# Optimization experiments

Hardware: AMD Instinct MI355X
Metric: run time of the kernel (lower is better)

## Reference

```python
import jax, jax.numpy as jnp
import numpy as np

H = 16        # num_heads
D = 128       # head_dim = hidden_size // num_heads
HID = 2048    # hidden_size
BLOCK = 64    # moba_chunk_size
TOPK = 8      # moba_topk


def setup_inputs() -> dict:
    key = jax.random.key(0)
    ks = jax.random.split(key, 5)
    B, S = 1, 2048
    hidden_states = jax.random.normal(ks[0], (B, S, HID), dtype=jnp.float32)
    scale = HID ** -0.5
    Wq = jax.random.normal(ks[1], (HID, H * D), dtype=jnp.float32) * scale
    Wk = jax.random.normal(ks[2], (HID, H * D), dtype=jnp.float32) * scale
    Wv = jax.random.normal(ks[3], (HID, H * D), dtype=jnp.float32) * scale
    Wo = jax.random.normal(ks[4], (H * D, HID), dtype=jnp.float32) * scale
    return {"hidden_states": hidden_states, "Wq": Wq, "Wk": Wk, "Wv": Wv, "Wo": Wo}


def _moba_forward(hidden_states, Wq, Wk, Wv, Wo):
    B, S, _ = hidden_states.shape
    nb = S // BLOCK
    INF = jnp.float32(jnp.inf)

    q = (hidden_states @ Wq).reshape(B, S, H, D)
    k = (hidden_states @ Wk).reshape(B, S, H, D)
    v = (hidden_states @ Wv).reshape(B, S, H, D)

    # MoBA gating: mean-pooled key per block -> [B, nb, H, D]
    kg = k.reshape(B, nb, BLOCK, H, D).mean(axis=2)
    gate = jnp.einsum('bshd,bnhd->bhsn', q, kg)  # [B,H,S,nb]

    pos = jnp.arange(S)
    qb = pos // BLOCK                 # query's own block
    blk = jnp.arange(nb)
    is_self = qb[:, None] == blk[None, :]                      # self block always selected
    not_past = pos[:, None] < (blk[None, :] + 1) * BLOCK       # blocks not fully in the past
    gate = jnp.where(is_self, INF, jnp.where(not_past, -INF, gate))

    kk = min(TOPK, nb)
    topv, topi = jax.lax.top_k(gate, kk)                       # [B,H,S,kk]
    thresh = topv.min(axis=-1, keepdims=True)
    idx_mask = (topi[..., None] == blk).any(axis=-2)           # [B,H,S,nb]
    need = (gate >= thresh) & idx_mask
    gate_bias = jnp.where(need, 0.0, -INF)                     # additive block mask

    sm_scale = D ** -0.5
    qk = jnp.einsum('bshd,bthd->bhst', q, k) * sm_scale        # [B,H,S,S]
    qk = qk.reshape(B, H, S, nb, BLOCK) + gate_bias[..., None]
    qk = qk.reshape(B, H, S, S)
    causal = pos[:, None] >= pos[None, :]
    qk = jnp.where(causal, qk, -INF)

    p = jax.nn.softmax(qk, axis=-1)
    o = jnp.einsum('bhst,bthd->bshd', p, v).reshape(B, S, H * D)
    return o @ Wo


def reference(hidden_states, Wq, Wk, Wv, Wo):
    # Returns (output, attentions=None, past_key_values=None) in the original;
    # only the output tensor matters for correctness.
    return _moba_forward(hidden_states, Wq, Wk, Wv, Wo)
```

## Files before the change

kernel.cpp:

```cpp
#include <hip/hip_runtime.h>
#include <hip/hip_bf16.h>
#include <stdint.h>
#include <stddef.h>


using bh = __bf16;
typedef __bf16 bhx8 __attribute__((ext_vector_type(8)));
typedef __bf16 bhx4 __attribute__((ext_vector_type(4)));
typedef float  f32x4 __attribute__((ext_vector_type(4)));

#define SEQ   2048
#define HIDN  2048
#define NHEAD 16
#define HDIM  128
#define NBLK  32
#define BLKSZ 64
#define NQKV  6144
#define NGATE 512
#define LDC   136
#define PSTRIDE ((size_t)SEQ * NGATE)

#define GLDS16(gsrc, ldst)                                                     \
  __builtin_amdgcn_global_load_lds(                                            \
      (const __attribute__((address_space(1))) uint32_t*)(gsrc),               \
      (__attribute__((address_space(3))) uint32_t*)(ldst), 16, 0, 0)

__global__ __launch_bounds__(256) void split_f32(const float* __restrict__ in,
                                                 bh* __restrict__ hi, bh* __restrict__ lo, int n) {
  int i = (blockIdx.x * 256 + threadIdx.x) * 4;
  if (i >= n) return;
  float4 v = *(const float4*)(in + i);
  bhx4 h4, l4;
  float vv[4] = {v.x, v.y, v.z, v.w};
#pragma unroll
  for (int e = 0; e < 4; e++) {
    bh h = (bh)vv[e];
    h4[e] = h;
    l4[e] = (bh)(vv[e] - (float)h);
  }
  *(bhx4*)(hi + i) = h4;
  *(bhx4*)(lo + i) = l4;
}

__global__ __launch_bounds__(256) void transpose_cast4(const float* __restrict__ Wq,
                                                       const float* __restrict__ Wk,
                                                       const float* __restrict__ Wv,
                                                       const float* __restrict__ Wo,
                                                       bh* __restrict__ wqkvT, bh* __restrict__ woT) {
  __shared__ float tile[32][33];
  const int z = blockIdx.z;
  const float* in = (z == 0) ? Wq : (z == 1) ? Wk : (z == 2) ? Wv : Wo;
  bh* out = (z < 3) ? (wqkvT + (size_t)z * HIDN * HIDN) : woT;
  int tx = threadIdx.x, ty = threadIdx.y;
  int c0 = blockIdx.x * 32, r0 = blockIdx.y * 32;
#pragma unroll
  for (int i = 0; i < 4; i++)
    tile[ty + i * 8][tx] = in[(size_t)(r0 + ty + i * 8) * HIDN + c0 + tx];
  __syncthreads();
#pragma unroll
  for (int i = 0; i < 4; i++)
    out[(size_t)(c0 + ty + i * 8) * HIDN + r0 + tx] = (bh)tile[tx][ty + i * 8];
}

#define GEMM_STAGE_TILE(SRC, r0_, ldsbase)                                       \
  {                                                                              \
    _Pragma("unroll")                                                            \
    for (int it_ = 0; it_ < 4; it_++) {                                          \
      int idx_ = it_ * 256 + t;                                                  \
      int row_ = idx_ >> 3, x_ = (idx_ & 7) << 4;                                \
      GLDS16((const char*)(SRC) + (size_t)(r0_ + row_) * strideB + kbyte +       \
                 (x_ ^ ((row_ & 7) << 4)),                                       \
             (char*)(ldsbase) + ((idx_ >> 6) << 10));                            \
    }                                                                            \
  }

__global__ __launch_bounds__(256) void gemm_bt(const bh* __restrict__ A, const bh* __restrict__ BT,
                                               bh* __restrict__ Cb, int M, int N, int K) {
  __shared__ __align__(16) bh smem[128 * LDC];
  bh* As = smem;
  bh* Bs = smem + 128 * 64;
  const int t = threadIdx.x;
  const int L = t & 63, w = t >> 6;
  const int wm = w & 1, wn = w >> 1;
  const int quad = L >> 4, lo = L & 15;
  const int m0 = blockIdx.y * 128, n0 = blockIdx.x * 128;
  const size_t strideB = (size_t)K * 2;

  f32x4 acc[4][4];
#pragma unroll
  for (int i = 0; i < 4; i++)
#pragma unroll
    for (int j = 0; j < 4; j++) acc[i][j] = (f32x4){0.f, 0.f, 0.f, 0.f};

  for (int k0 = 0; k0 < K; k0 += 64) {
    const size_t kbyte = (size_t)k0 * 2;
    GEMM_STAGE_TILE(A, m0, As);
    GEMM_STAGE_TILE(BT, n0, Bs);
    __syncthreads();
#pragma unroll
    for (int ks = 0; ks < 2; ks++) {
      bhx8 af[4], bf_[4];
#pragma unroll
      for (int i = 0; i < 4; i++) {
        const int row = wm * 64 + i * 16 + lo;
        af[i] = *(const bhx8*)((const char*)As + row * 128 +
                               ((ks * 64 + quad * 16) ^ ((row & 7) << 4)));
      }
#pragma unroll
      for (int j = 0; j < 4; j++) {
        const int row = wn * 64 + j * 16 + lo;
        bf_[j] = *(const bhx8*)((const char*)Bs + row * 128 +
                                ((ks * 64 + quad * 16) ^ ((row & 7) << 4)));
      }
#pragma unroll
      for (int i = 0; i < 4; i++)
#pragma unroll
        for (int j = 0; j < 4; j++)
          acc[i][j] = __builtin_amdgcn_mfma_f32_16x16x32_bf16(af[i], bf_[j], acc[i][j], 0, 0, 0);
    }
    __syncthreads();
  }

  bh* Cs = smem;
#pragma unroll
  for (int i = 0; i < 4; i++)
#pragma unroll
    for (int j = 0; j < 4; j++)
#pragma unroll
      for (int r = 0; r < 4; r++)
        Cs[(wm * 64 + i * 16 + quad * 4 + r) * LDC + wn * 64 + j * 16 + lo] = (bh)acc[i][j][r];
  __syncthreads();
#pragma unroll
  for (int it = 0; it < 8; it++) {
    int idx = it * 256 + t;
    int row = idx >> 4, cg = idx & 15;
    *(uint4*)(Cb + (size_t)(m0 + row) * N + n0 + cg * 8) = *(const uint4*)&Cs[row * LDC + cg * 8];
  }
}

__global__ __launch_bounds__(256) void gemm_bt128f(const bh* __restrict__ A, const bh* __restrict__ BT,
                                                   float* __restrict__ Cf, int M, int N, int K) {
  __shared__ __align__(16) bh smem[2 * 128 * 64];
  bh* As = smem;
  bh* Bs = smem + 128 * 64;
  const int t = threadIdx.x;
  const int L = t & 63, w = t >> 6;
  const int wm = w & 1, wn = w >> 1;
  const int quad = L >> 4, lo = L & 15;
  const int m0 = blockIdx.y * 128, n0 = blockIdx.x * 128;
  const size_t strideB = (size_t)K * 2;

  f32x4 acc[4][4];
#pragma unroll
  for (int i = 0; i < 4; i++)
#pragma unroll
    for (int j = 0; j < 4; j++) acc[i][j] = (f32x4){0.f, 0.f, 0.f, 0.f};

  for (int k0 = 0; k0 < K; k0 += 64) {
    const size_t kbyte = (size_t)k0 * 2;
    GEMM_STAGE_TILE(A, m0, As);
    GEMM_STAGE_TILE(BT, n0, Bs);
    __syncthreads();
#pragma unroll
    for (int ks = 0; ks < 2; ks++) {
      bhx8 af[4], bf_[4];
#pragma unroll
      for (int i = 0; i < 4; i++) {
        const int row = wm * 64 + i * 16 + lo;
        af[i] = *(const bhx8*)((const char*)As + row * 128 +
                               ((ks * 64 + quad * 16) ^ ((row & 7) << 4)));
      }
#pragma unroll
      for (int j = 0; j < 4; j++) {
        const int row = wn * 64 + j * 16 + lo;
        bf_[j] = *(const bhx8*)((const char*)Bs + row * 128 +
                                ((ks * 64 + quad * 16) ^ ((row & 7) << 4)));
      }
#pragma unroll
      for (int i = 0; i < 4; i++)
#pragma unroll
        for (int j = 0; j < 4; j++)
          acc[i][j] = __builtin_amdgcn_mfma_f32_16x16x32_bf16(af[i], bf_[j], acc[i][j], 0, 0, 0);
    }
    __syncthreads();
  }

#pragma unroll
  for (int i = 0; i < 4; i++)
#pragma unroll
    for (int j = 0; j < 4; j++)
#pragma unroll
      for (int r = 0; r < 4; r++) {
        int row = m0 + wm * 64 + i * 16 + quad * 4 + r;
        int col = n0 + wn * 64 + j * 16 + lo;
        Cf[(size_t)row * N + col] = acc[i][j][r];
      }
}

__global__ __launch_bounds__(256) void gemm_gate_split(const bh* __restrict__ hs_hi,
                                                       const bh* __restrict__ hs_lo,
                                                       const bh* __restrict__ wg_hi,
                                                       const bh* __restrict__ wg_lo,
                                                       float* __restrict__ part) {
  __shared__ __align__(16) bh smem[2 * 128 * 64];
  bh* As = smem;
  bh* Bs = smem + 128 * 64;
  const int t = threadIdx.x;
  const int L = t & 63, w = t >> 6;
  const int wm = w & 1, wn = w >> 1;
  const int quad = L >> 4, lo = L & 15;
  const int m0 = blockIdx.y * 128, n0 = blockIdx.x * 128;
  const int z = blockIdx.z;
  const bh* Ap = ((z >> 1) == 1) ? hs_lo : hs_hi;
  const bh* Bp = ((z >> 1) == 2) ? wg_lo : wg_hi;
  const int kb = (z & 1) * 1024;
  const size_t strideB = (size_t)HIDN * 2;

  f32x4 acc[4][4];
#pragma unroll
  for (int i = 0; i < 4; i++)
#pragma unroll
    for (int j = 0; j < 4; j++) acc[i][j] = (f32x4){0.f, 0.f, 0.f, 0.f};

  for (int k0 = 0; k0 < 1024; k0 += 64) {
    const size_t kbyte = (size_t)(kb + k0) * 2;
    GEMM_STAGE_TILE(Ap, m0, As);
    GEMM_STAGE_TILE(Bp, n0, Bs);
    __syncthreads();
#pragma unroll
    for (int ks = 0; ks < 2; ks++) {
      bhx8 af[4], bf_[4];
#pragma unroll
      for (int i = 0; i < 4; i++) {
        const int row = wm * 64 + i * 16 + lo;
        af[i] = *(const bhx8*)((const char*)As + row * 128 +
                               ((ks * 64 + quad * 16) ^ ((row & 7) << 4)));
      }
#pragma unroll
      for (int j = 0; j < 4; j++) {
        const int row = wn * 64 + j * 16 + lo;
        bf_[j] = *(const bhx8*)((const char*)Bs + row * 128 +
                                ((ks * 64 + quad * 16) ^ ((row & 7) << 4)));
      }
#pragma unroll
      for (int i = 0; i < 4; i++)
#pragma unroll
        for (int j = 0; j < 4; j++)
          acc[i][j] = __builtin_amdgcn_mfma_f32_16x16x32_bf16(af[i], bf_[j], acc[i][j], 0, 0, 0);
    }
    __syncthreads();
  }

#pragma unroll
  for (int i = 0; i < 4; i++)
#pragma unroll
    for (int j = 0; j < 4; j++)
#pragma unroll
      for (int r = 0; r < 4; r++) {
        int row = m0 + wm * 64 + i * 16 + quad * 4 + r;
        int col = n0 + wn * 64 + j * 16 + lo;
        part[(size_t)z * PSTRIDE + (size_t)row * NGATE + col] = acc[i][j][r];
      }
}

__global__ __launch_bounds__(256) void hsmean_k(const float* __restrict__ hs, float* __restrict__ hsm) {
  int idx = blockIdx.x * 256 + threadIdx.x;
  int n = idx >> 11, c = idx & 2047;
  const float* p = hs + (size_t)(n * BLKSZ) * HIDN + c;
  float s = 0.f;
#pragma unroll 8
  for (int r = 0; r < BLKSZ; r++) s += p[(size_t)r * HIDN];
  hsm[idx] = s * (1.0f / 64.0f);
}

__global__ __launch_bounds__(256) void kg_partial(const float* __restrict__ hsm,
                                                  const float* __restrict__ Wk,
                                                  float* __restrict__ part) {
  __shared__ float hl[32][256];
  int c = blockIdx.x * 256 + threadIdx.x;
  int k0 = blockIdx.y * 256;
#pragma unroll 4
  for (int i = 0; i < 32; i++) hl[i][threadIdx.x] = hsm[(size_t)i * HIDN + k0 + threadIdx.x];
  __syncthreads();
  float acc[32];
#pragma unroll
  for (int n = 0; n < 32; n++) acc[n] = 0.f;
  for (int k4 = 0; k4 < 64; k4++) {
    float w0 = Wk[(size_t)(k0 + k4 * 4 + 0) * HIDN + c];
    float w1 = Wk[(size_t)(k0 + k4 * 4 + 1) * HIDN + c];
    float w2 = Wk[(size_t)(k0 + k4 * 4 + 2) * HIDN + c];
    float w3 = Wk[(size_t)(k0 + k4 * 4 + 3) * HIDN + c];
#pragma unroll
    for (int n = 0; n < 32; n++) {
      float4 hv = *(const float4*)&hl[n][k4 * 4];
      acc[n] += hv.x * w0 + hv.y * w1 + hv.z * w2 + hv.w * w3;
    }
  }
#pragma unroll
  for (int n = 0; n < 32; n++)
    part[((size_t)blockIdx.y * 32 + n) * HIDN + c] = acc[n];
}

__global__ __launch_bounds__(256) void kg_reduce8(const float* __restrict__ part, float* __restrict__ kg) {
  int idx = blockIdx.x * 256 + threadIdx.x;
  float s = 0.f;
#pragma unroll
  for (int kc = 0; kc < 8; kc++) s += part[(size_t)kc * 65536 + idx];
  kg[idx] = s;
}

__global__ __launch_bounds__(256) void wg_k(const float* __restrict__ Wq, const float* __restrict__ kg,
                                            float* __restrict__ wg) {
  __shared__ float kl[32][128];
  int h = blockIdx.y;
  int r = blockIdx.x * 256 + threadIdx.x;
  for (int i = threadIdx.x; i < 32 * 128; i += 256)
    kl[i >> 7][i & 127] = kg[(size_t)(i >> 7) * HIDN + h * HDIM + (i & 127)];
  __syncthreads();
  float acc[32];
#pragma unroll
  for (int n = 0; n < 32; n++) acc[n] = 0.f;
  const float4* wrow = (const float4*)(Wq + (size_t)r * HIDN + h * HDIM);
  for (int d4 = 0; d4 < 32; d4++) {
    float4 w = wrow[d4];
#pragma unroll
    for (int n = 0; n < 32; n++) {
      float4 kv = *(const float4*)&kl[n][d4 * 4];
      acc[n] += w.x * kv.x + w.y * kv.y + w.z * kv.z + w.w * kv.w;
    }
  }
#pragma unroll
  for (int n = 0; n < 32; n++)
    wg[(size_t)(h * 32 + n) * HIDN + r] = acc[n];
}

__global__ __launch_bounds__(256) void gate_topk(const float* __restrict__ part,
                                                 unsigned* __restrict__ bsel) {
  int w = threadIdx.x >> 6, L = threadIdx.x & 63;
  int p = blockIdx.x * 4 + w;
  int h = p >> 11, s = p & 2047;
  int qb = s >> 6;
  int n = L;
  float g = -1e30f;
  if (n == qb) g = 1e30f;
  else if (n < qb) {
    size_t off = (size_t)s * NGATE + h * 32 + n;
    g = part[off] + part[off + PSTRIDE] + part[off + 2 * PSTRIDE] +
        part[off + 3 * PSTRIDE] + part[off + 4 * PSTRIDE] + part[off + 5 * PSTRIDE];
  }
  int rank = 0;
#pragma unroll
  for (int j = 0; j < 32; j++) {
    float gj = __shfl(g, j, 64);
    if (gj > g || (gj == g && j < n)) rank++;
  }
  bool sel = (n <= qb) && (n < 32) && (rank < 8);
  unsigned long long bm = __ballot(sel);
  if (L == 0) bsel[p] = (unsigned)(bm & 0xffffffffull);
}

__global__ __launch_bounds__(256) void vtrans(const bh* __restrict__ qkv, bh* __restrict__ vt) {
  __shared__ float tile[32][33];
  int tx = threadIdx.x, ty = threadIdx.y;
  int s0 = blockIdx.x * 32, d0 = blockIdx.y * 32, h = blockIdx.z;
#pragma unroll
  for (int i = 0; i < 4; i++)
    tile[ty + i * 8][tx] = (float)qkv[(size_t)(s0 + ty + i * 8) * NQKV + 2 * HIDN + h * HDIM + d0 + tx];
  __syncthreads();
#pragma unroll
  for (int i = 0; i < 4; i++)
    vt[((size_t)h * HDIM + d0 + ty + i * 8) * SEQ + s0 + tx] = (bh)tile[tx][ty + i * 8];
}

__global__ __launch_bounds__(256) void attn(const bh* __restrict__ qkv, const bh* __restrict__ vt,
                                            const unsigned* __restrict__ bsel, bh* __restrict__ obuf) {
  __shared__ __align__(16) bh Ksm[2][64 * 128];
  __shared__ __align__(16) bh Vsm[2][128 * 64];
  __shared__ __align__(16) bh PLb[4][16 * 72];
  __shared__ unsigned ublk;
  const int t = threadIdx.x;
  const int w = t >> 6, L = t & 63;
  const int quad = L >> 4, lo = L & 15;
  const int bid = blockIdx.x;
  const int jj = bid >> 3;
  const int h = ((bid & 7) << 1) | (jj & 1);
  const int qb = (jj < 32) ? (31 - (jj >> 1)) : ((jj - 32) >> 1);
  const int s0 = qb * 64 + w * 16;

  unsigned bs[4];
#pragma unroll
  for (int r = 0; r < 4; r++) bs[r] = bsel[h * SEQ + s0 + quad * 4 + r];
  unsigned uni = bs[0] | bs[1] | bs[2] | bs[3];
  uni |= (unsigned)__shfl_xor((int)uni, 16);
  uni |= (unsigned)__shfl_xor((int)uni, 32);
  const unsigned uniw = uni;
  if (t == 0) ublk = 0;
  __syncthreads();
  if (L == 0) atomicOr(&ublk, uni);
  __syncthreads();
  const unsigned un = ublk;

  bhx8 aq[4];
  const bh* qrow = qkv + (size_t)(s0 + lo) * NQKV + h * HDIM;
#pragma unroll
  for (int ks = 0; ks < 4; ks++) aq[ks] = *(const bhx8*)(qrow + ks * 32 + quad * 8);

  f32x4 oacc[8];
#pragma unroll
  for (int j = 0; j < 8; j++) oacc[j] = (f32x4){0.f, 0.f, 0.f, 0.f};
  f32x4 lacc = (f32x4){0.f, 0.f, 0.f, 0.f};
  float mi[4] = {-1e30f, -1e30f, -1e30f, -1e30f};

  bhx8 ones8;
#pragma unroll
  for (int e = 0; e < 8; e++) ones8[e] = (bh)1.0f;

  const float scale = 0.08838834764831845f;

  auto stageKV = [&](int b, int n) {
    const char* ksrc = (const char*)(qkv + (size_t)(n * BLKSZ) * NQKV + HIDN + h * HDIM);
    const char* vsrc = (const char*)(vt + ((size_t)h * HDIM) * SEQ + n * BLKSZ);
    char* kb = (char*)&Ksm[b][0];
    char* vb = (char*)&Vsm[b][0];
#pragma unroll
    for (int it = 0; it < 4; it++) {
      int idx = it * 256 + t;
      int row = idx >> 4, x = (idx & 15) << 4;
      GLDS16(ksrc + (size_t)row * (NQKV * 2) + (x ^ ((row & 7) << 4)),
             kb + ((idx >> 6) << 10));
    }
#pragma unroll
    for (int it = 0; it < 4; it++) {
      int idx = it * 256 + t;
      int row = idx >> 3, x = (idx & 7) << 4;
      GLDS16(vsrc + (size_t)row * (SEQ * 2) + (x ^ ((row & 7) << 4)),
             vb + ((idx >> 6) << 10));
    }
  };

  unsigned rem = un;
  int ncur = (int)__builtin_ctz(rem);
  rem &= rem - 1;
  stageKV(0, ncur);
  int cur = 0;

  while (true) {
    int nnext = -1;
    if (rem) { nnext = (int)__builtin_ctz(rem); rem &= rem - 1; }
    if (nnext >= 0) {
      stageKV(cur ^ 1, nnext);
      asm volatile("s_waitcnt vmcnt(8)" ::: "memory");
    } else {
      asm volatile("s_waitcnt vmcnt(0)" ::: "memory");
    }
    __builtin_amdgcn_s_barrier();

    if ((uniw >> ncur) & 1) {
      const char* Kc = (const char*)&Ksm[cur][0];
      const char* Vc = (const char*)&Vsm[cur][0];
      const bool self = (ncur == qb);

      f32x4 sc[4];
      __builtin_amdgcn_s_setprio(1);
#pragma unroll
      for (int nt = 0; nt < 4; nt++) {
        f32x4 s4 = (f32x4){0.f, 0.f, 0.f, 0.f};
#pragma unroll
        for (int ks = 0; ks < 4; ks++) {
          const int row = nt * 16 + lo;
          bhx8 bk = *(const bhx8*)(Kc + row * 256 + ((ks * 64 + quad * 16) ^ ((row & 7) << 4)));
          s4 = __builtin_amdgcn_mfma_f32_16x16x32_bf16(aq[ks], bk, s4, 0, 0, 0);
        }
        sc[nt] = s4;
      }
      __builtin_amdgcn_s_setprio(0);

      if (self) {
#pragma unroll
        for (int nt = 0; nt < 4; nt++)
#pragma unroll
          for (int r = 0; r < 4; r++) {
            float v = sc[nt][r] * scale;
            int kpos = ncur * BLKSZ + nt * 16 + lo;
            int qpos = s0 + quad * 4 + r;
            bool ok = ((bs[r] >> ncur) & 1) && (kpos <= qpos);
            sc[nt][r] = ok ? v : -1e30f;
          }
      } else {
        float bias[4];
#pragma unroll
        for (int r = 0; r < 4; r++)
          bias[r] = ((bs[r] >> ncur) & 1) ? 0.f : -1e30f;
#pragma unroll
        for (int nt = 0; nt < 4; nt++)
#pragma unroll
          for (int r = 0; r < 4; r++)
            sc[nt][r] = sc[nt][r] * scale + bias[r];
      }
      float rm[4];
#pragma unroll
      for (int r = 0; r < 4; r++)
        rm[r] = fmaxf(fmaxf(sc[0][r], sc[1][r]), fmaxf(sc[2][r], sc[3][r]));
#pragma unroll
      for (int off = 1; off < 16; off <<= 1)
#pragma unroll
        for (int r = 0; r < 4; r++) rm[r] = fmaxf(rm[r], __shfl_xor(rm[r], off));

      bool exceed = (rm[0] > mi[0] + 8.f) || (rm[1] > mi[1] + 8.f) ||
                    (rm[2] > mi[2] + 8.f) || (rm[3] > mi[3] + 8.f);
      if (__any(exceed)) {
        float alpha[4];
#pragma unroll
        for (int r = 0; r < 4; r++) {
          float nm = fmaxf(mi[r], rm[r]);
          alpha[r] = __expf(mi[r] - nm);
          mi[r] = nm;
        }
#pragma unroll
        for (int j = 0; j < 8; j++)
#pragma unroll
          for (int r = 0; r < 4; r++) oacc[j][r] *= alpha[r];
#pragma unroll
        for (int r = 0; r < 4; r++) lacc[r] *= alpha[r];
      }

#pragma unroll
      for (int nt = 0; nt < 4; nt++)
#pragma unroll
        for (int r = 0; r < 4; r++) {
          float sv = sc[nt][r];
          float pv = (sv > -1e29f) ? __expf(sv - mi[r]) : 0.f;
          PLb[w][(quad * 4 + r) * 72 + nt * 16 + lo] = (bh)pv;
        }

      __builtin_amdgcn_s_setprio(1);
#pragma unroll
      for (int kk = 0; kk < 2; kk++) {
        bhx8 pa = *(const bhx8*)&PLb[w][lo * 72 + kk * 32 + quad * 8];
        lacc = __builtin_amdgcn_mfma_f32_16x16x32_bf16(pa, ones8, lacc, 0, 0, 0);
#pragma unroll
        for (int j = 0; j < 8; j++) {
          const int row = j * 16 + lo;
          bhx8 vv = *(const bhx8*)(Vc + row * 128 + ((kk * 64 + quad * 16) ^ ((row & 7) << 4)));
          oacc[j] = __builtin_amdgcn_mfma_f32_16x16x32_bf16(pa, vv, oacc[j], 0, 0, 0);
        }
      }
      __builtin_amdgcn_s_setprio(0);
    }

    __builtin_amdgcn_s_barrier();
    if (nnext < 0) break;
    ncur = nnext;
    cur ^= 1;
  }

#pragma unroll
  for (int j = 0; j < 8; j++)
#pragma unroll
    for (int r = 0; r < 4; r++) {
      int row = s0 + quad * 4 + r;
      int col = h * HDIM + j * 16 + lo;
      obuf[(size_t)row * HIDN + col] = (bh)(oacc[j][r] / lacc[r]);
    }
}

extern "C" void kernel_launch(void* const* d_in, const int* in_sizes, int n_in,
                              void* d_out, int out_size, void* d_ws, size_t ws_size,
                              hipStream_t stream) {
  const float* hs = (const float*)d_in[0];
  const float* Wq = (const float*)d_in[1];
  const float* Wk = (const float*)d_in[2];
  const float* Wv = (const float*)d_in[3];
  const float* Wo = (const float*)d_in[4];

  char* ws = (char*)d_ws;
  bh* hs_hi = (bh*)ws;            ws += (size_t)SEQ * HIDN * 2;
  bh* hs_lo = (bh*)ws;            ws += (size_t)SEQ * HIDN * 2;
  bh* wqkvT = (bh*)ws;            ws += (size_t)NQKV * HIDN * 2;
  bh* woT = (bh*)ws;              ws += (size_t)HIDN * HIDN * 2;
  bh* qkv = (bh*)ws;              ws += (size_t)SEQ * NQKV * 2;
  bh* vt = (bh*)ws;               ws += (size_t)NHEAD * HDIM * SEQ * 2;
  bh* obuf = (bh*)ws;             ws += (size_t)SEQ * HIDN * 2;
  float* hsm = (float*)ws;        ws += (size_t)NBLK * HIDN * 4;
  float* kg_part = (float*)ws;    ws += (size_t)8 * NBLK * HIDN * 4;
  float* kg = (float*)ws;         ws += (size_t)NBLK * HIDN * 4;
  float* wg = (float*)ws;         ws += (size_t)NGATE * HIDN * 4;
  bh* wg_hi = (bh*)ws;            ws += (size_t)NGATE * HIDN * 2;
  bh* wg_lo = (bh*)ws;            ws += (size_t)NGATE * HIDN * 2;
  unsigned* bsel = (unsigned*)ws; ws += (size_t)NHEAD * SEQ * 4;
  float* gpart = (float*)wqkvT;

  split_f32<<<(SEQ * HIDN) / 1024, 256, 0, stream>>>(hs, hs_hi, hs_lo, SEQ * HIDN);
  transpose_cast4<<<dim3(64, 64, 4), dim3(32, 8), 0, stream>>>(Wq, Wk, Wv, Wo, wqkvT, woT);

  gemm_bt<<<dim3(NQKV / 128, SEQ / 128), 256, 0, stream>>>(hs_hi, wqkvT, qkv, SEQ, NQKV, HIDN);

  hsmean_k<<<(NBLK * HIDN) / 256, 256, 0, stream>>>(hs, hsm);
  kg_partial<<<dim3(8, 8), 256, 0, stream>>>(hsm, Wk, kg_part);
  kg_reduce8<<<(NBLK * HIDN) / 256, 256, 0, stream>>>(kg_part, kg);
  wg_k<<<dim3(8, NHEAD), 256, 0, stream>>>(Wq, kg, wg);
  split_f32<<<(NGATE * HIDN) / 1024, 256, 0, stream>>>(wg, wg_hi, wg_lo, NGATE * HIDN);
  gemm_gate_split<<<dim3(NGATE / 128, SEQ / 128, 6), 256, 0, stream>>>(hs_hi, hs_lo, wg_hi, wg_lo, gpart);
  gate_topk<<<(NHEAD * SEQ) / 4, 256, 0, stream>>>(gpart, bsel);

  vtrans<<<dim3(SEQ / 32, HDIM / 32, NHEAD), dim3(32, 8), 0, stream>>>(qkv, vt);
  attn<<<dim3(NBLK * NHEAD), 256, 0, stream>>>(qkv, vt, bsel, obuf);

  gemm_bt128f<<<dim3(HIDN / 128, SEQ / 128), 256, 0, stream>>>(obuf, woT, (float*)d_out, SEQ, HIDN, HIDN);
}
```

Measured before the change: 469.3 us.

## Merge QKV GEMM with finer-split kg partial into one heterogeneous launch

```diff
diff --git a/kernel.cpp b/kernel.cpp
--- a/kernel.cpp
+++ b/kernel.cpp
@@ -74,67 +74,101 @@
     }                                                                            \
   }
 
-__global__ __launch_bounds__(256) void gemm_bt(const bh* __restrict__ A, const bh* __restrict__ BT,
-                                               bh* __restrict__ Cb, int M, int N, int K) {
-  __shared__ __align__(16) bh smem[128 * LDC];
-  bh* As = smem;
-  bh* Bs = smem + 128 * 64;
+__global__ __launch_bounds__(256) void qkvkg(const bh* __restrict__ A, const bh* __restrict__ BT,
+                                             bh* __restrict__ Cb,
+                                             const float* __restrict__ hsm,
+                                             const float* __restrict__ Wk,
+                                             float* __restrict__ part) {
+  __shared__ __align__(16) char smraw[128 * LDC * 2];
   const int t = threadIdx.x;
-  const int L = t & 63, w = t >> 6;
-  const int wm = w & 1, wn = w >> 1;
-  const int quad = L >> 4, lo = L & 15;
-  const int m0 = blockIdx.y * 128, n0 = blockIdx.x * 128;
-  const size_t strideB = (size_t)K * 2;
-
-  f32x4 acc[4][4];
-#pragma unroll
-  for (int i = 0; i < 4; i++)
-#pragma unroll
-    for (int j = 0; j < 4; j++) acc[i][j] = (f32x4){0.f, 0.f, 0.f, 0.f};
-
-  for (int k0 = 0; k0 < K; k0 += 64) {
-    const size_t kbyte = (size_t)k0 * 2;
-    GEMM_STAGE_TILE(A, m0, As);
-    GEMM_STAGE_TILE(BT, n0, Bs);
+
+  if (blockIdx.x < 768) {
+    bh* smem = (bh*)smraw;
+    bh* As = smem;
+    bh* Bs = smem + 128 * 64;
+    const int L = t & 63, w = t >> 6;
+    const int wm = w & 1, wn = w >> 1;
+    const int quad = L >> 4, lo = L & 15;
+    const int m0 = (blockIdx.x / 48) * 128, n0 = (blockIdx.x % 48) * 128;
+    const size_t strideB = (size_t)HIDN * 2;
+
+    f32x4 acc[4][4];
+#pragma unroll
+    for (int i = 0; i < 4; i++)
+#pragma unroll
+      for (int j = 0; j < 4; j++) acc[i][j] = (f32x4){0.f, 0.f, 0.f, 0.f};
+
+    for (int k0 = 0; k0 < HIDN; k0 += 64) {
+      const size_t kbyte = (size_t)k0 * 2;
+      GEMM_STAGE_TILE(A, m0, As);
+      GEMM_STAGE_TILE(BT, n0, Bs);
+      __syncthreads();
+#pragma unroll
+      for (int ks = 0; ks < 2; ks++) {
+        bhx8 af[4], bf_[4];
+#pragma unroll
+        for (int i = 0; i < 4; i++) {
+          const int row = wm * 64 + i * 16 + lo;
+          af[i] = *(const bhx8*)((const char*)As + row * 128 +
+                                 ((ks * 64 + quad * 16) ^ ((row & 7) << 4)));
+        }
+#pragma unroll
+        for (int j = 0; j < 4; j++) {
+          const int row = wn * 64 + j * 16 + lo;
+          bf_[j] = *(const bhx8*)((const char*)Bs + row * 128 +
+                                  ((ks * 64 + quad * 16) ^ ((row & 7) << 4)));
+        }
+#pragma unroll
+        for (int i = 0; i < 4; i++)
+#pragma unroll
+          for (int j = 0; j < 4; j++)
+            acc[i][j] = __builtin_amdgcn_mfma_f32_16x16x32_bf16(af[i], bf_[j], acc[i][j], 0, 0, 0);
+      }
+      __syncthreads();
+    }
+
+    bh* Cs = smem;
+#pragma unroll
+    for (int i = 0; i < 4; i++)
+#pragma unroll
+      for (int j = 0; j < 4; j++)
+#pragma unroll
+        for (int r = 0; r < 4; r++)
+          Cs[(wm * 64 + i * 16 + quad * 4 + r) * LDC + wn * 64 + j * 16 + lo] = (bh)acc[i][j][r];
     __syncthreads();
 #pragma unroll
-    for (int ks = 0; ks < 2; ks++) {
-      bhx8 af[4], bf_[4];
-#pragma unroll
-      for (int i = 0; i < 4; i++) {
-        const int row = wm * 64 + i * 16 + lo;
-        af[i] = *(const bhx8*)((const char*)As + row * 128 +
-                               ((ks * 64 + quad * 16) ^ ((row & 7) << 4)));
-      }
-#pragma unroll
-      for (int j = 0; j < 4; j++) {
-        const int row = wn * 64 + j * 16 + lo;
-        bf_[j] = *(const bhx8*)((const char*)Bs + row * 128 +
-                                ((ks * 64 + quad * 16) ^ ((row & 7) << 4)));
-      }
-#pragma unroll
-      for (int i = 0; i < 4; i++)
-#pragma unroll
-        for (int j = 0; j < 4; j++)
-          acc[i][j] = __builtin_amdgcn_mfma_f32_16x16x32_bf16(af[i], bf_[j], acc[i][j], 0, 0, 0);
-    }
+    for (int it = 0; it < 8; it++) {
+      int idx = it * 256 + t;
+      int row = idx >> 4, cg = idx & 15;
+      *(uint4*)(Cb + (size_t)(m0 + row) * NQKV + n0 + cg * 8) = *(const uint4*)&Cs[row * LDC + cg * 8];
+    }
+  } else {
+    float (*hl)[32] = (float (*)[32])smraw;
+    const int b2 = blockIdx.x - 768;
+    const int c = (b2 & 7) * 256 + t;
+    const int ky = b2 >> 3;
+    const int k0 = ky * 32;
+    for (int i = t; i < 32 * 32; i += 256)
+      hl[i >> 5][i & 31] = hsm[(size_t)(i >> 5) * HIDN + k0 + (i & 31)];
     __syncthreads();
-  }
-
-  bh* Cs = smem;
-#pragma unroll
-  for (int i = 0; i < 4; i++)
-#pragma unroll
-    for (int j = 0; j < 4; j++)
-#pragma unroll
-      for (int r = 0; r < 4; r++)
-        Cs[(wm * 64 + i * 16 + quad * 4 + r) * LDC + wn * 64 + j * 16 + lo] = (bh)acc[i][j][r];
-  __syncthreads();
-#pragma unroll
-  for (int it = 0; it < 8; it++) {
-    int idx = it * 256 + t;
-    int row = idx >> 4, cg = idx & 15;
-    *(uint4*)(Cb + (size_t)(m0 + row) * N + n0 + cg * 8) = *(const uint4*)&Cs[row * LDC + cg * 8];
+    float acc[32];
+#pragma unroll
+    for (int n = 0; n < 32; n++) acc[n] = 0.f;
+#pragma unroll 2
+    for (int k4 = 0; k4 < 8; k4++) {
+      float w0 = Wk[(size_t)(k0 + k4 * 4 + 0) * HIDN + c];
+      float w1 = Wk[(size_t)(k0 + k4 * 4 + 1) * HIDN + c];
+      float w2 = Wk[(size_t)(k0 + k4 * 4 + 2) * HIDN + c];
+      float w3 = Wk[(size_t)(k0 + k4 * 4 + 3) * HIDN + c];
+#pragma unroll
+      for (int n = 0; n < 32; n++) {
+        float4 hv = *(const float4*)&hl[n][k4 * 4];
+        acc[n] += hv.x * w0 + hv.y * w1 + hv.z * w2 + hv.w * w3;
+      }
+    }
+#pragma unroll
+    for (int n = 0; n < 32; n++)
+      part[((size_t)ky * 32 + n) * HIDN + c] = acc[n];
   }
 }
 
@@ -273,39 +307,11 @@
   hsm[idx] = s * (1.0f / 64.0f);
 }
 
-__global__ __launch_bounds__(256) void kg_partial(const float* __restrict__ hsm,
-                                                  const float* __restrict__ Wk,
-                                                  float* __restrict__ part) {
-  __shared__ float hl[32][256];
-  int c = blockIdx.x * 256 + threadIdx.x;
-  int k0 = blockIdx.y * 256;
-#pragma unroll 4
-  for (int i = 0; i < 32; i++) hl[i][threadIdx.x] = hsm[(size_t)i * HIDN + k0 + threadIdx.x];
-  __syncthreads();
-  float acc[32];
-#pragma unroll
-  for (int n = 0; n < 32; n++) acc[n] = 0.f;
-  for (int k4 = 0; k4 < 64; k4++) {
-    float w0 = Wk[(size_t)(k0 + k4 * 4 + 0) * HIDN + c];
-    float w1 = Wk[(size_t)(k0 + k4 * 4 + 1) * HIDN + c];
-    float w2 = Wk[(size_t)(k0 + k4 * 4 + 2) * HIDN + c];
-    float w3 = Wk[(size_t)(k0 + k4 * 4 + 3) * HIDN + c];
-#pragma unroll
-    for (int n = 0; n < 32; n++) {
-      float4 hv = *(const float4*)&hl[n][k4 * 4];
-      acc[n] += hv.x * w0 + hv.y * w1 + hv.z * w2 + hv.w * w3;
-    }
-  }
-#pragma unroll
-  for (int n = 0; n < 32; n++)
-    part[((size_t)blockIdx.y * 32 + n) * HIDN + c] = acc[n];
-}
-
-__global__ __launch_bounds__(256) void kg_reduce8(const float* __restrict__ part, float* __restrict__ kg) {
+__global__ __launch_bounds__(256) void kg_reduce64(const float* __restrict__ part, float* __restrict__ kg) {
   int idx = blockIdx.x * 256 + threadIdx.x;
   float s = 0.f;
 #pragma unroll
-  for (int kc = 0; kc < 8; kc++) s += part[(size_t)kc * 65536 + idx];
+  for (int kc = 0; kc < 64; kc++) s += part[(size_t)kc * 65536 + idx];
   kg[idx] = s;
 }
 
@@ -528,8 +534,7 @@
       for (int nt = 0; nt < 4; nt++)
 #pragma unroll
         for (int r = 0; r < 4; r++) {
-          float sv = sc[nt][r];
-          float pv = (sv > -1e29f) ? __expf(sv - mi[r]) : 0.f;
+          float pv = __expf(sc[nt][r] - mi[r]);
           PLb[w][(quad * 4 + r) * 72 + nt * 16 + lo] = (bh)pv;
         }
 
@@ -582,22 +587,21 @@
   bh* vt = (bh*)ws;               ws += (size_t)NHEAD * HDIM * SEQ * 2;
   bh* obuf = (bh*)ws;             ws += (size_t)SEQ * HIDN * 2;
   float* hsm = (float*)ws;        ws += (size_t)NBLK * HIDN * 4;
-  float* kg_part = (float*)ws;    ws += (size_t)8 * NBLK * HIDN * 4;
   float* kg = (float*)ws;         ws += (size_t)NBLK * HIDN * 4;
   float* wg = (float*)ws;         ws += (size_t)NGATE * HIDN * 4;
   bh* wg_hi = (bh*)ws;            ws += (size_t)NGATE * HIDN * 2;
   bh* wg_lo = (bh*)ws;            ws += (size_t)NGATE * HIDN * 2;
   unsigned* bsel = (unsigned*)ws; ws += (size_t)NHEAD * SEQ * 4;
+  float* kg_part = (float*)vt;
   float* gpart = (float*)wqkvT;
 
   split_f32<<<(SEQ * HIDN) / 1024, 256, 0, stream>>>(hs, hs_hi, hs_lo, SEQ * HIDN);
   transpose_cast4<<<dim3(64, 64, 4), dim3(32, 8), 0, stream>>>(Wq, Wk, Wv, Wo, wqkvT, woT);
-
-  gemm_bt<<<dim3(NQKV / 128, SEQ / 128), 256, 0, stream>>>(hs_hi, wqkvT, qkv, SEQ, NQKV, HIDN);
-
   hsmean_k<<<(NBLK * HIDN) / 256, 256, 0, stream>>>(hs, hsm);
-  kg_partial<<<dim3(8, 8), 256, 0, stream>>>(hsm, Wk, kg_part);
-  kg_reduce8<<<(NBLK * HIDN) / 256, 256, 0, stream>>>(kg_part, kg);
+
+  qkvkg<<<768 + 512, 256, 0, stream>>>(hs_hi, wqkvT, qkv, hsm, Wk, kg_part);
+
+  kg_reduce64<<<(NBLK * HIDN) / 256, 256, 0, stream>>>(kg_part, kg);
   wg_k<<<dim3(8, NHEAD), 256, 0, stream>>>(Wq, kg, wg);
   split_f32<<<(NGATE * HIDN) / 1024, 256, 0, stream>>>(wg, wg_hi, wg_lo, NGATE * HIDN);
   gemm_gate_split<<<dim3(NGATE / 128, SEQ / 128, 6), 256, 0, stream>>>(hs_hi, hs_lo, wg_hi, wg_lo, gpart);
```

Result: faster. 421.1 us (-10.3%).
